# Kernel tuning notes

Hardware: AMD Instinct MI355X
Metric: run time of the kernel (lower is better)

Reference implementation:

```python
import math
import jax, jax.numpy as jnp
import numpy as np

FEATURES = 512
ATTACK_TIME = 0.005
RELEASE_TIME = 0.05
DELTA_T = 0.001
ATTACK_COEFF = 1.0 - math.exp(-DELTA_T / ATTACK_TIME)
RELEASE_COEFF = 1.0 - math.exp(-DELTA_T / RELEASE_TIME)


def setup_inputs() -> dict:
    key = jax.random.key(0)
    x = jax.random.normal(key, (8, 16384, FEATURES), dtype=jnp.float32)
    return {"x": x}


def reference(x) -> jnp.ndarray:
    # x: [batch, seq, features]; recurrence along seq (dim=1).
    B, T, F = x.shape
    a = jnp.asarray(ATTACK_COEFF, x.dtype)
    r = jnp.asarray(RELEASE_COEFF, x.dtype)

    def step(y_prev, x_t):
        # y_prev, x_t: [batch, features]
        diff_mask = (x_t - y_prev > 0).astype(x_t.dtype)  # gt0
        alpha = diff_mask * a + (1 - diff_mask) * r
        y = alpha * x_t + (1 - alpha) * y_prev
        return y, y

    y0 = jnp.zeros((B, F), dtype=x.dtype)
    _, ys = jax.lax.scan(step, y0, jnp.swapaxes(x, 0, 1))  # ys: [seq, batch, features]
    return jnp.swapaxes(ys, 0, 1)
```

## Files before the change

### kernel.cpp

```cpp
#include <hip/hip_runtime.h>


typedef float v4 __attribute__((ext_vector_type(4)));

#define T_LEN   16384
#define F_DIM   512
#define FV      128
#define SEGS    16
#define SEG_LEN 1024
#define WARM    384
#define UNROLL  8

#define ATTACK_C  0.18126924692201818f
#define RELEASE_C 0.019801326696744665f

__device__ __forceinline__ float astep(float x, float y) {
    float d = x - y;
    float alpha = (d > 0.0f) ? ATTACK_C : RELEASE_C;
    return fmaf(alpha, d, y);
}

__global__ __launch_bounds__(64) void arema_kernel(const float* __restrict__ xg,
                                                   float* __restrict__ yg) {
    const int f4 = blockIdx.x * 64 + threadIdx.x;
    const int s  = blockIdx.y;
    const int b  = blockIdx.z;

    const int sL    = s * SEG_LEN;
    const int begin = (s == 0) ? 0 : (sL - WARM);
    const int end   = sL + SEG_LEN;

    const v4* __restrict__ xin = (const v4*)xg + (size_t)b * T_LEN * FV + f4;
    v4* __restrict__ yout      = (v4*)yg       + (size_t)b * T_LEN * FV + f4;

    float y0 = 0.f, y1 = 0.f, y2 = 0.f, y3 = 0.f;
    v4 bufA[UNROLL], bufB[UNROLL];

    int t = begin;
#pragma unroll
    for (int i = 0; i < UNROLL; ++i)
        bufA[i] = xin[(size_t)(t + i) * FV];

    const int nch = (end - begin) / UNROLL;

    for (int c = 0; c < nch; c += 2) {
#pragma unroll
        for (int i = 0; i < UNROLL; ++i)
            bufB[i] = xin[(size_t)(t + UNROLL + i) * FV];

        {
            const bool wr = (t >= sL);
#pragma unroll
            for (int i = 0; i < UNROLL; ++i) {
                v4 xv = bufA[i];
                y0 = astep(xv.x, y0);
                y1 = astep(xv.y, y1);
                y2 = astep(xv.z, y2);
                y3 = astep(xv.w, y3);
                if (wr) {
                    v4 o = {y0, y1, y2, y3};
                    __builtin_nontemporal_store(o, &yout[(size_t)(t + i) * FV]);
                }
            }
        }

        const int tp = (c + 2 < nch) ? (t + 2 * UNROLL) : begin;
#pragma unroll
        for (int i = 0; i < UNROLL; ++i)
            bufA[i] = xin[(size_t)(tp + i) * FV];

        {
            const int tb = t + UNROLL;
            const bool wr = (tb >= sL);
#pragma unroll
            for (int i = 0; i < UNROLL; ++i) {
                v4 xv = bufB[i];
                y0 = astep(xv.x, y0);
                y1 = astep(xv.y, y1);
                y2 = astep(xv.z, y2);
                y3 = astep(xv.w, y3);
                if (wr) {
                    v4 o = {y0, y1, y2, y3};
                    __builtin_nontemporal_store(o, &yout[(size_t)(tb + i) * FV]);
                }
            }
        }

        t += 2 * UNROLL;
    }
}

extern "C" void kernel_launch(void* const* d_in, const int* in_sizes, int n_in,
                              void* d_out, int out_size, void* d_ws, size_t ws_size,
                              hipStream_t stream) {
    const float* x = (const float*)d_in[0];
    float* y = (float*)d_out;
    const int B = in_sizes[0] / (T_LEN * F_DIM);
    dim3 grid(FV / 64, SEGS, B);
    arema_kernel<<<grid, dim3(64, 1, 1), 0, stream>>>(x, y);
}
```

Baseline: 572.7 us.

## Use scalar per-thread features and more, shorter segments for higher occupancy

After: 461.9 us. -19.3%, faster.

```diff
diff --git a/kernel.cpp b/kernel.cpp
--- a/kernel.cpp
+++ b/kernel.cpp
@@ -1,15 +1,12 @@
 #include <hip/hip_runtime.h>
 
 
-typedef float v4 __attribute__((ext_vector_type(4)));
-
 #define T_LEN   16384
 #define F_DIM   512
-#define FV      128
-#define SEGS    16
-#define SEG_LEN 1024
-#define WARM    384
-#define UNROLL  8
+#define SEGS    32
+#define SEG_LEN 512
+#define WARM    256
+#define UNROLL  16
 
 #define ATTACK_C  0.18126924692201818f
 #define RELEASE_C 0.019801326696744665f
@@ -20,69 +17,57 @@
     return fmaf(alpha, d, y);
 }
 
-__global__ __launch_bounds__(64) void arema_kernel(const float* __restrict__ xg,
-                                                   float* __restrict__ yg) {
-    const int f4 = blockIdx.x * 64 + threadIdx.x;
-    const int s  = blockIdx.y;
-    const int b  = blockIdx.z;
+__global__ __launch_bounds__(256) void arema_kernel(const float* __restrict__ xg,
+                                                    float* __restrict__ yg) {
+    const int f = blockIdx.x * 256 + threadIdx.x;
+    const int s = blockIdx.y;
+    const int b = blockIdx.z;
 
     const int sL    = s * SEG_LEN;
     const int begin = (s == 0) ? 0 : (sL - WARM);
     const int end   = sL + SEG_LEN;
 
-    const v4* __restrict__ xin = (const v4*)xg + (size_t)b * T_LEN * FV + f4;
-    v4* __restrict__ yout      = (v4*)yg       + (size_t)b * T_LEN * FV + f4;
+    const float* __restrict__ xin = xg + (size_t)b * T_LEN * F_DIM + f;
+    float* __restrict__ yout      = yg + (size_t)b * T_LEN * F_DIM + f;
 
-    float y0 = 0.f, y1 = 0.f, y2 = 0.f, y3 = 0.f;
-    v4 bufA[UNROLL], bufB[UNROLL];
+    float y = 0.f;
+    float bufA[UNROLL], bufB[UNROLL];
 
     int t = begin;
 #pragma unroll
     for (int i = 0; i < UNROLL; ++i)
-        bufA[i] = xin[(size_t)(t + i) * FV];
+        bufA[i] = xin[(size_t)(t + i) * F_DIM];
 
     const int nch = (end - begin) / UNROLL;
 
     for (int c = 0; c < nch; c += 2) {
 #pragma unroll
         for (int i = 0; i < UNROLL; ++i)
-            bufB[i] = xin[(size_t)(t + UNROLL + i) * FV];
+            bufB[i] = xin[(size_t)(t + UNROLL + i) * F_DIM];
 
         {
             const bool wr = (t >= sL);
 #pragma unroll
             for (int i = 0; i < UNROLL; ++i) {
-                v4 xv = bufA[i];
-                y0 = astep(xv.x, y0);
-                y1 = astep(xv.y, y1);
-                y2 = astep(xv.z, y2);
-                y3 = astep(xv.w, y3);
-                if (wr) {
-                    v4 o = {y0, y1, y2, y3};
-                    __builtin_nontemporal_store(o, &yout[(size_t)(t + i) * FV]);
-                }
+                y = astep(bufA[i], y);
+                if (wr)
+                    __builtin_nontemporal_store(y, &yout[(size_t)(t + i) * F_DIM]);
             }
         }
 
         const int tp = (c + 2 < nch) ? (t + 2 * UNROLL) : begin;
 #pragma unroll
         for (int i = 0; i < UNROLL; ++i)
-            bufA[i] = xin[(size_t)(tp + i) * FV];
+            bufA[i] = xin[(size_t)(tp + i) * F_DIM];
 
         {
             const int tb = t + UNROLL;
             const bool wr = (tb >= sL);
 #pragma unroll
             for (int i = 0; i < UNROLL; ++i) {
-                v4 xv = bufB[i];
-                y0 = astep(xv.x, y0);
-                y1 = astep(xv.y, y1);
-                y2 = astep(xv.z, y2);
-                y3 = astep(xv.w, y3);
-                if (wr) {
-                    v4 o = {y0, y1, y2, y3};
-                    __builtin_nontemporal_store(o, &yout[(size_t)(tb + i) * FV]);
-                }
+                y = astep(bufB[i], y);
+                if (wr)
+                    __builtin_nontemporal_store(y, &yout[(size_t)(tb + i) * F_DIM]);
             }
         }
 
@@ -96,6 +81,6 @@
     const float* x = (const float*)d_in[0];
     float* y = (float*)d_out;
     const int B = in_sizes[0] / (T_LEN * F_DIM);
-    dim3 grid(FV / 64, SEGS, B);
-    arema_kernel<<<grid, dim3(64, 1, 1), 0, stream>>>(x, y);
+    dim3 grid(F_DIM / 256, SEGS, B);
+    arema_kernel<<<grid, dim3(256, 1, 1), 0, stream>>>(x, y);
 }
```
